# Kernel tuning notes

Measured on AMD Instinct MI355X. Metric: run time of the kernel, lower is better.

## Reference

```python
import math
import jax, jax.numpy as jnp
import numpy as np

D_MODEL = 1024
N_HEADS = 16
D_HEAD = D_MODEL // N_HEADS


def setup_inputs() -> dict:
    key = jax.random.key(0)
    kx, kqkv, ko = jax.random.split(key, 3)
    B, T = 4, 2048
    x = jax.random.normal(kx, (B, T, D_MODEL), dtype=jnp.float32)
    # Linear(d_model, 3*d_model, bias=False): weight stored as [out, in]
    s = 1.0 / math.sqrt(D_MODEL)
    W_qkv = jax.random.uniform(kqkv, (3 * D_MODEL, D_MODEL), dtype=jnp.float32, minval=-s, maxval=s)
    W_o = jax.random.uniform(ko, (D_MODEL, D_MODEL), dtype=jnp.float32, minval=-s, maxval=s)
    return {"x": x, "W_qkv": W_qkv, "W_o": W_o}


def reference(x, W_qkv, W_o):
    B, T, C = x.shape
    H, Dh = N_HEADS, D_HEAD
    qkv = jnp.einsum('btc,oc->bto', x, W_qkv)            # [B,T,3C]
    qkv = qkv.reshape(B, T, 3, H, Dh)
    q = jnp.transpose(qkv[:, :, 0], (0, 2, 1, 3))        # [B,H,T,Dh]
    k = jnp.transpose(qkv[:, :, 1], (0, 2, 1, 3))
    v = jnp.transpose(qkv[:, :, 2], (0, 2, 1, 3))
    scale = 1.0 / math.sqrt(Dh)
    attn = jnp.einsum('bhqd,bhkd->bhqk', q, k) * scale   # [B,H,T,T]
    causal = jnp.tril(jnp.ones((T, T), dtype=bool))
    attn = jnp.where(causal, attn, -jnp.inf)
    attn = jax.nn.softmax(attn, axis=-1)
    out = jnp.einsum('bhqk,bhkd->bhqd', attn, v)         # [B,H,T,Dh]
    out = jnp.transpose(out, (0, 2, 1, 3)).reshape(B, T, C)
    return jnp.einsum('btc,oc->bto', out, W_o)
```

## Files before the change

kernel.cpp:

```cpp
#include <hip/hip_runtime.h>
#include <hip/hip_bf16.h>
#include <cstdint>

#define TT      2048
#define NBATCH  4
#define BTROWS  8192
#define CDIM    1024
#define NQKV    3072
#define QSCALE  0.18033688011112042f

using bf16x8 = __attribute__((ext_vector_type(8))) short;
using f32x4  = __attribute__((ext_vector_type(4))) float;
using f32x16 = __attribute__((ext_vector_type(16))) float;

#define GLOAD_LDS16(g, l)                                                     \
  __builtin_amdgcn_global_load_lds(                                           \
      (const __attribute__((address_space(1))) unsigned int*)(g),             \
      (__attribute__((address_space(3))) unsigned int*)(l), 16, 0, 0)

__device__ inline short f2bf(float f) {
  unsigned u = __builtin_bit_cast(unsigned, f);
  u += 0x7FFF + ((u >> 16) & 1);
  return (short)(u >> 16);
}

__global__ __launch_bounds__(256) void conv_bf16(const float* __restrict__ in,
                                                 short* __restrict__ out, int n) {
  int i = (blockIdx.x * 256 + threadIdx.x) * 4;
  if (i + 3 < n) {
    float4 v = *(const float4*)(in + i);
    short4 o;
    o.x = f2bf(v.x); o.y = f2bf(v.y); o.z = f2bf(v.z); o.w = f2bf(v.w);
    *(short4*)(out + i) = o;
  }
}

__global__ __launch_bounds__(256) void gemm_qkv(const short* __restrict__ A,
                                                const short* __restrict__ Bw,
                                                short* __restrict__ Qb,
                                                short* __restrict__ Kb,
                                                short* __restrict__ Vb) {
  const int K = CDIM;
  __shared__ __attribute__((aligned(16))) short As[128 * 32];
  __shared__ __attribute__((aligned(16))) short Bs[128 * 32];
  int tid = threadIdx.x;
  int bid = blockIdx.x;
  int bm = ((bid & 7) << 3) | (bid >> 3);
  int bn = blockIdx.y;
  int lane = tid & 63, wid = tid >> 6;
  int wr = wid >> 1, wc = wid & 1;
  int la = lane & 15, lg = lane >> 4;

  const short* Ab = A + (size_t)bm * 128 * K;
  const short* Bb = Bw + (size_t)bn * 128 * K;

  f32x4 acc[4][4];
#pragma unroll
  for (int m = 0; m < 4; m++)
#pragma unroll
    for (int n = 0; n < 4; n++) acc[m][n] = (f32x4){0.f, 0.f, 0.f, 0.f};

  int c0 = tid, c1 = tid + 256;
  for (int k0 = 0; k0 < K; k0 += 32) {
    GLOAD_LDS16(Ab + (c0 >> 2) * K + k0 + (c0 & 3) * 8, &As[c0 * 8]);
    GLOAD_LDS16(Ab + (c1 >> 2) * K + k0 + (c1 & 3) * 8, &As[c1 * 8]);
    GLOAD_LDS16(Bb + (c0 >> 2) * K + k0 + (c0 & 3) * 8, &Bs[c0 * 8]);
    GLOAD_LDS16(Bb + (c1 >> 2) * K + k0 + (c1 & 3) * 8, &Bs[c1 * 8]);
    __syncthreads();
    bf16x8 af[4], bfr[4];
#pragma unroll
    for (int m = 0; m < 4; m++)
      af[m] = *(const bf16x8*)&As[(wr * 64 + m * 16 + la) * 32 + lg * 8];
#pragma unroll
    for (int n = 0; n < 4; n++)
      bfr[n] = *(const bf16x8*)&Bs[(wc * 64 + n * 16 + la) * 32 + lg * 8];
#pragma unroll
    for (int m = 0; m < 4; m++)
#pragma unroll
      for (int n = 0; n < 4; n++)
        acc[m][n] = __builtin_amdgcn_mfma_f32_16x16x32_bf16(af[m], bfr[n],
                                                            acc[m][n], 0, 0, 0);
    __syncthreads();
  }

#pragma unroll
  for (int m = 0; m < 4; m++) {
    int rbase = bm * 128 + wr * 64 + m * 16 + lg * 4;
    int b = rbase >> 11;
    int tb = rbase & 2047;
#pragma unroll
    for (int n = 0; n < 4; n++) {
      int col = bn * 128 + wc * 64 + n * 16 + la;
      int which = col >> 10;
      int h = (col >> 6) & 15;
      int d = col & 63;
      if (which == 2) {
        short4 o4;
        o4.x = f2bf(acc[m][n][0]); o4.y = f2bf(acc[m][n][1]);
        o4.z = f2bf(acc[m][n][2]); o4.w = f2bf(acc[m][n][3]);
        *(short4*)&Vb[((size_t)(b * 16 + h) * 64 + d) * TT + tb] = o4;
      } else {
        short* dst = (which == 0) ? Qb : Kb;
        float sc = (which == 0) ? QSCALE : 1.0f;
        size_t base = ((size_t)(b * 16 + h) * TT) * 64 + d;
#pragma unroll
        for (int r = 0; r < 4; r++)
          dst[base + (size_t)(tb + r) * 64] = f2bf(acc[m][n][r] * sc);
      }
    }
  }
}

__global__ __launch_bounds__(256, 3) void attn_fwd2(const short* __restrict__ Qb,
                                                    const short* __restrict__ Kb,
                                                    const short* __restrict__ Vtg,
                                                    short* __restrict__ Ob) {
  __shared__ __attribute__((aligned(16))) short lds[10240];
  short* Ks = lds;
  short* Vs = lds + 4096;

  int tid = threadIdx.x, lane = tid & 63, w = tid >> 6;
  int l31 = lane & 31, hi = lane >> 5, l7 = lane & 7;
  int gid = blockIdx.x;
  int qt = 15 - (gid & 15);
  int bh = gid >> 4;
  int q0 = qt * 128;
  int qw = q0 + w * 32;
  int qg = qw + l31;

  const short* Qh = Qb + (size_t)bh * TT * 64;
  const short* Kh = Kb + (size_t)bh * TT * 64;
  const short* Vh = Vtg + (size_t)bh * 64 * TT;

  bf16x8 q[4];
#pragma unroll
  for (int c = 0; c < 4; c++)
    q[c] = *(const bf16x8*)(Qh + (size_t)qg * 64 + c * 16 + hi * 8);

  f32x16 o0, o1;
#pragma unroll
  for (int r = 0; r < 16; r++) { o0[r] = 0.f; o1[r] = 0.f; }
  float m = -1e30f, lsum = 0.f;

  int nt = 2 * qt + 2;
  int c0 = tid, c1 = tid + 256;
  int r0 = c0 >> 3, cc0 = c0 & 7;
  int r1 = c1 >> 3, cc1 = c1 & 7;

  bf16x8 kr0, kr1, vr0, vr1;
  kr0 = *(const bf16x8*)(Kh + (size_t)r0 * 64 + cc0 * 8);
  kr1 = *(const bf16x8*)(Kh + (size_t)r1 * 64 + cc1 * 8);
  vr0 = *(const bf16x8*)(Vh + (size_t)r0 * TT + cc0 * 8);
  vr1 = *(const bf16x8*)(Vh + (size_t)r1 * TT + cc1 * 8);

  for (int it = 0; it < nt; it++) {
    int kv0 = it * 64;
    __syncthreads();
    *(bf16x8*)&Ks[r0 * 64 + ((cc0 ^ (r0 & 7)) * 8)] = kr0;
    *(bf16x8*)&Ks[r1 * 64 + ((cc1 ^ (r1 & 7)) * 8)] = kr1;
    *(bf16x8*)&Vs[r0 * 64 + ((cc0 ^ (r0 & 7)) * 8)] = vr0;
    *(bf16x8*)&Vs[r1 * 64 + ((cc1 ^ (r1 & 7)) * 8)] = vr1;
    __syncthreads();
    if (it + 1 < nt) {
      int kn = kv0 + 64;
      kr0 = *(const bf16x8*)(Kh + (size_t)(kn + r0) * 64 + cc0 * 8);
      kr1 = *(const bf16x8*)(Kh + (size_t)(kn + r1) * 64 + cc1 * 8);
      vr0 = *(const bf16x8*)(Vh + (size_t)r0 * TT + kn + cc0 * 8);
      vr1 = *(const bf16x8*)(Vh + (size_t)r1 * TT + kn + cc1 * 8);
    }
    if (kv0 <= qw + 31) {
      f32x16 st0, st1;
#pragma unroll
      for (int r = 0; r < 16; r++) { st0[r] = 0.f; st1[r] = 0.f; }
#pragma unroll
      for (int c = 0; c < 4; c++) {
        int cc = c * 2 + hi;
        bf16x8 kf0 = *(const bf16x8*)&Ks[l31 * 64 + ((cc ^ l7) * 8)];
        bf16x8 kf1 = *(const bf16x8*)&Ks[(32 + l31) * 64 + ((cc ^ l7) * 8)];
        st0 = __builtin_amdgcn_mfma_f32_32x32x16_bf16(kf0, q[c], st0, 0, 0, 0);
        st1 = __builtin_amdgcn_mfma_f32_32x32x16_bf16(kf1, q[c], st1, 0, 0, 0);
      }
      if (kv0 + 63 > qw) {
#pragma unroll
        for (int r = 0; r < 16; r++) {
          int kloc = (r & 3) + 8 * (r >> 2) + 4 * hi;
          if (kv0 + kloc > qg)      st0[r] = -1e30f;
          if (kv0 + 32 + kloc > qg) st1[r] = -1e30f;
        }
      }
      float tm[16];
#pragma unroll
      for (int r = 0; r < 16; r++) tm[r] = fmaxf(st0[r], st1[r]);
#pragma unroll
      for (int s = 8; s >= 1; s >>= 1)
#pragma unroll
        for (int r = 0; r < 16; r++)
          if (r < s) tm[r] = fmaxf(tm[r], tm[r + s]);
      float pm = tm[0];
      pm = fmaxf(pm, __shfl_xor(pm, 32));
      if (!__all(pm <= m + 8.f)) {
        float mn = fmaxf(m, pm);
        float fac = exp2f(m - mn);
        lsum *= fac;
#pragma unroll
        for (int r = 0; r < 16; r++) { o0[r] *= fac; o1[r] *= fac; }
        m = mn;
      }
      float ts[16];
#pragma unroll
      for (int r = 0; r < 16; r++) {
        st0[r] = exp2f(st0[r] - m);
        st1[r] = exp2f(st1[r] - m);
        ts[r] = st0[r] + st1[r];
      }
#pragma unroll
      for (int s = 8; s >= 1; s >>= 1)
#pragma unroll
        for (int r = 0; r < 16; r++)
          if (r < s) ts[r] += ts[r + s];
      float rs = ts[0];
      rs += __shfl_xor(rs, 32);
      lsum += rs;
#pragma unroll
      for (int kb = 0; kb < 2; kb++) {
#pragma unroll
        for (int c2 = 0; c2 < 2; c2++) {
          float p0 = kb ? st1[8 * c2 + 0] : st0[8 * c2 + 0];
          float p1 = kb ? st1[8 * c2 + 1] : st0[8 * c2 + 1];
          float p2 = kb ? st1[8 * c2 + 2] : st0[8 * c2 + 2];
          float p3 = kb ? st1[8 * c2 + 3] : st0[8 * c2 + 3];
          float p4 = kb ? st1[8 * c2 + 4] : st0[8 * c2 + 4];
          float p5 = kb ? st1[8 * c2 + 5] : st0[8 * c2 + 5];
          float p6 = kb ? st1[8 * c2 + 6] : st0[8 * c2 + 6];
          float p7 = kb ? st1[8 * c2 + 7] : st0[8 * c2 + 7];
          unsigned u0, u1, u2, u3;
          asm("v_cvt_pk_bf16_f32 %0, %1, %2" : "=v"(u0) : "v"(p0), "v"(p1));
          asm("v_cvt_pk_bf16_f32 %0, %1, %2" : "=v"(u1) : "v"(p2), "v"(p3));
          asm("v_cvt_pk_bf16_f32 %0, %1, %2" : "=v"(u2) : "v"(p4), "v"(p5));
          asm("v_cvt_pk_bf16_f32 %0, %1, %2" : "=v"(u3) : "v"(p6), "v"(p7));
          asm volatile("v_permlane32_swap_b32 %0, %1" : "+v"(u0), "+v"(u2));
          asm volatile("v_permlane32_swap_b32 %0, %1" : "+v"(u1), "+v"(u3));
          union { unsigned u[4]; bf16x8 v; } pa;
          pa.u[0] = u0; pa.u[1] = u1; pa.u[2] = u2; pa.u[3] = u3;
          int ccv = kb * 4 + c2 * 2 + hi;
          bf16x8 vf0 = *(const bf16x8*)&Vs[l31 * 64 + ((ccv ^ l7) * 8)];
          bf16x8 vf1 = *(const bf16x8*)&Vs[(32 + l31) * 64 + ((ccv ^ l7) * 8)];
          o0 = __builtin_amdgcn_mfma_f32_32x32x16_bf16(vf0, pa.v, o0, 0, 0, 0);
          o1 = __builtin_amdgcn_mfma_f32_32x32x16_bf16(vf1, pa.v, o1, 0, 0, 0);
        }
      }
    }
  }

  __syncthreads();
  short* Os = lds + w * (32 * 80);
  float inv = 1.f / lsum;
#pragma unroll
  for (int k = 0; k < 4; k++) {
    float a0 = o0[4 * k + 0] * inv, a1 = o0[4 * k + 1] * inv;
    float a2 = o0[4 * k + 2] * inv, a3 = o0[4 * k + 3] * inv;
    float b0 = o1[4 * k + 0] * inv, b1 = o1[4 * k + 1] * inv;
    float b2 = o1[4 * k + 2] * inv, b3 = o1[4 * k + 3] * inv;
    unsigned w0, w1, w2, w3;
    asm("v_cvt_pk_bf16_f32 %0, %1, %2" : "=v"(w0) : "v"(a0), "v"(a1));
    asm("v_cvt_pk_bf16_f32 %0, %1, %2" : "=v"(w1) : "v"(a2), "v"(a3));
    asm("v_cvt_pk_bf16_f32 %0, %1, %2" : "=v"(w2) : "v"(b0), "v"(b1));
    asm("v_cvt_pk_bf16_f32 %0, %1, %2" : "=v"(w3) : "v"(b2), "v"(b3));
    int d = 8 * k + 4 * hi;
    uint2 pa; pa.x = w0; pa.y = w1;
    uint2 pb; pb.x = w2; pb.y = w3;
    *(uint2*)&Os[l31 * 80 + d] = pa;
    *(uint2*)&Os[l31 * 80 + 32 + d] = pb;
  }
  __syncthreads();
  int b = bh >> 4, h = bh & 15;
#pragma unroll
  for (int pass = 0; pass < 4; pass++) {
    int qr = pass * 8 + (lane >> 3);
    int cc = lane & 7;
    bf16x8 v = *(const bf16x8*)&Os[qr * 80 + cc * 8];
    *(bf16x8*)&Ob[((size_t)(b * TT + q0 + w * 32 + qr)) * CDIM + h * 64 + cc * 8] = v;
  }
}

__global__ __launch_bounds__(256) void gemm_out(const short* __restrict__ A,
                                                const short* __restrict__ Bw,
                                                float* __restrict__ C) {
  const int K = CDIM;
  __shared__ __attribute__((aligned(16))) short As[128 * 32];
  __shared__ __attribute__((aligned(16))) short Bs[128 * 32];
  int tid = threadIdx.x;
  int bid = blockIdx.x;
  int bm = ((bid & 7) << 3) | (bid >> 3);
  int bn = blockIdx.y;
  int lane = tid & 63, wid = tid >> 6;
  int wr = wid >> 1, wc = wid & 1;
  int la = lane & 15, lg = lane >> 4;

  const short* Ab = A + (size_t)bm * 128 * K;
  const short* Bb = Bw + (size_t)bn * 128 * K;

  f32x4 acc[4][4];
#pragma unroll
  for (int m = 0; m < 4; m++)
#pragma unroll
    for (int n = 0; n < 4; n++) acc[m][n] = (f32x4){0.f, 0.f, 0.f, 0.f};

  int c0 = tid, c1 = tid + 256;
  for (int k0 = 0; k0 < K; k0 += 32) {
    GLOAD_LDS16(Ab + (c0 >> 2) * K + k0 + (c0 & 3) * 8, &As[c0 * 8]);
    GLOAD_LDS16(Ab + (c1 >> 2) * K + k0 + (c1 & 3) * 8, &As[c1 * 8]);
    GLOAD_LDS16(Bb + (c0 >> 2) * K + k0 + (c0 & 3) * 8, &Bs[c0 * 8]);
    GLOAD_LDS16(Bb + (c1 >> 2) * K + k0 + (c1 & 3) * 8, &Bs[c1 * 8]);
    __syncthreads();
    bf16x8 af[4], bfr[4];
#pragma unroll
    for (int m = 0; m < 4; m++)
      af[m] = *(const bf16x8*)&As[(wr * 64 + m * 16 + la) * 32 + lg * 8];
#pragma unroll
    for (int n = 0; n < 4; n++)
      bfr[n] = *(const bf16x8*)&Bs[(wc * 64 + n * 16 + la) * 32 + lg * 8];
#pragma unroll
    for (int m = 0; m < 4; m++)
#pragma unroll
      for (int n = 0; n < 4; n++)
        acc[m][n] = __builtin_amdgcn_mfma_f32_16x16x32_bf16(af[m], bfr[n],
                                                            acc[m][n], 0, 0, 0);
    __syncthreads();
  }

#pragma unroll
  for (int m = 0; m < 4; m++) {
    int rbase = bm * 128 + wr * 64 + m * 16 + lg * 4;
#pragma unroll
    for (int n = 0; n < 4; n++) {
      int col = bn * 128 + wc * 64 + n * 16 + la;
#pragma unroll
      for (int r = 0; r < 4; r++)
        C[(size_t)(rbase + r) * CDIM + col] = acc[m][n][r];
    }
  }
}

extern "C" void kernel_launch(void* const* d_in, const int* in_sizes, int n_in,
                              void* d_out, int out_size, void* d_ws, size_t ws_size,
                              hipStream_t stream) {
  const float* x    = (const float*)d_in[0];
  const float* wqkv = (const float*)d_in[1];
  const float* wo   = (const float*)d_in[2];
  float* out = (float*)d_out;

  char* ws = (char*)d_ws;
  short* xb  = (short*)(ws);
  short* wqb = (short*)(ws + (size_t)(16 << 20));
  short* wob = (short*)(ws + (size_t)(22 << 20));
  short* Qb  = (short*)(ws + (size_t)(24 << 20));
  short* Kb  = (short*)(ws + (size_t)(40 << 20));
  short* Vb  = (short*)(ws + (size_t)(56 << 20));
  short* Ob  = (short*)(ws + (size_t)(72 << 20));

  conv_bf16<<<8192, 256, 0, stream>>>(x, xb, BTROWS * CDIM);
  conv_bf16<<<3072, 256, 0, stream>>>(wqkv, wqb, NQKV * CDIM);
  conv_bf16<<<1024, 256, 0, stream>>>(wo, wob, CDIM * CDIM);

  gemm_qkv<<<dim3(BTROWS / 128, NQKV / 128), 256, 0, stream>>>(xb, wqb, Qb, Kb, Vb);
  attn_fwd2<<<NBATCH * 16 * (TT / 128), 256, 0, stream>>>(Qb, Kb, Vb, Ob);
  gemm_out<<<dim3(BTROWS / 128, CDIM / 128), 256, 0, stream>>>(Ob, wob, out);
}
```

Measured before the change: 310.1 us.

## Stage Q/K epilogue through LDS for coalesced stores; raise MFMA wave priority

```diff
diff --git a/kernel.cpp b/kernel.cpp
--- a/kernel.cpp
+++ b/kernel.cpp
@@ -41,8 +41,9 @@
                                                 short* __restrict__ Kb,
                                                 short* __restrict__ Vb) {
   const int K = CDIM;
-  __shared__ __attribute__((aligned(16))) short As[128 * 32];
-  __shared__ __attribute__((aligned(16))) short Bs[128 * 32];
+  __shared__ __attribute__((aligned(16))) short smem[8192];
+  short* As = smem;
+  short* Bs = smem + 4096;
   int tid = threadIdx.x;
   int bid = blockIdx.x;
   int bm = ((bid & 7) << 3) | (bid >> 3);
@@ -83,30 +84,46 @@
     __syncthreads();
   }
 
-#pragma unroll
-  for (int m = 0; m < 4; m++) {
-    int rbase = bm * 128 + wr * 64 + m * 16 + lg * 4;
-    int b = rbase >> 11;
-    int tb = rbase & 2047;
-#pragma unroll
-    for (int n = 0; n < 4; n++) {
-      int col = bn * 128 + wc * 64 + n * 16 + la;
-      int which = col >> 10;
-      int h = (col >> 6) & 15;
-      int d = col & 63;
-      if (which == 2) {
+  int colbase = bn * 128 + wc * 64;
+  int which = colbase >> 10;
+  int b = bm >> 4;
+
+  if (which == 2) {
+#pragma unroll
+    for (int m = 0; m < 4; m++) {
+      int tb = (bm * 128 + wr * 64 + m * 16 + lg * 4) & 2047;
+#pragma unroll
+      for (int n = 0; n < 4; n++) {
+        int col = colbase + n * 16 + la;
+        int h = (col >> 6) & 15;
+        int d = col & 63;
         short4 o4;
         o4.x = f2bf(acc[m][n][0]); o4.y = f2bf(acc[m][n][1]);
         o4.z = f2bf(acc[m][n][2]); o4.w = f2bf(acc[m][n][3]);
         *(short4*)&Vb[((size_t)(b * 16 + h) * 64 + d) * TT + tb] = o4;
-      } else {
-        short* dst = (which == 0) ? Qb : Kb;
-        float sc = (which == 0) ? QSCALE : 1.0f;
-        size_t base = ((size_t)(b * 16 + h) * TT) * 64 + d;
+      }
+    }
+  } else {
+    short* dst = (which == 0) ? Qb : Kb;
+    float sc = (which == 0) ? QSCALE : 1.0f;
+    int h = (colbase >> 6) & 15;
+    size_t hbase = ((size_t)(b * 16 + h) * TT) * 64;
+    short* Ls = smem + wid * (16 * 72);
+    int rrow = lane & 15, chunk = lane >> 4;
+#pragma unroll
+    for (int m = 0; m < 4; m++) {
+#pragma unroll
+      for (int n = 0; n < 4; n++)
 #pragma unroll
         for (int r = 0; r < 4; r++)
-          dst[base + (size_t)(tb + r) * 64] = f2bf(acc[m][n][r] * sc);
-      }
+          Ls[(lg * 4 + r) * 72 + n * 16 + la] = f2bf(acc[m][n][r] * sc);
+      __syncthreads();
+      int t = (bm * 128 + wr * 64 + m * 16 + rrow) & 2047;
+      bf16x8 v0 = *(const bf16x8*)&Ls[rrow * 72 + chunk * 16];
+      bf16x8 v1 = *(const bf16x8*)&Ls[rrow * 72 + chunk * 16 + 8];
+      *(bf16x8*)&dst[hbase + (size_t)t * 64 + chunk * 16] = v0;
+      *(bf16x8*)&dst[hbase + (size_t)t * 64 + chunk * 16 + 8] = v1;
+      __syncthreads();
     }
   }
 }
@@ -172,6 +189,7 @@
       f32x16 st0, st1;
 #pragma unroll
       for (int r = 0; r < 16; r++) { st0[r] = 0.f; st1[r] = 0.f; }
+      __builtin_amdgcn_s_setprio(1);
 #pragma unroll
       for (int c = 0; c < 4; c++) {
         int cc = c * 2 + hi;
@@ -180,6 +198,7 @@
         st0 = __builtin_amdgcn_mfma_f32_32x32x16_bf16(kf0, q[c], st0, 0, 0, 0);
         st1 = __builtin_amdgcn_mfma_f32_32x32x16_bf16(kf1, q[c], st1, 0, 0, 0);
       }
+      __builtin_amdgcn_s_setprio(0);
       if (kv0 + 63 > qw) {
 #pragma unroll
         for (int r = 0; r < 16; r++) {
@@ -221,6 +240,7 @@
       float rs = ts[0];
       rs += __shfl_xor(rs, 32);
       lsum += rs;
+      __builtin_amdgcn_s_setprio(1);
 #pragma unroll
       for (int kb = 0; kb < 2; kb++) {
 #pragma unroll
@@ -249,6 +269,7 @@
           o1 = __builtin_amdgcn_mfma_f32_32x32x16_bf16(vf1, pa.v, o1, 0, 0, 0);
         }
       }
+      __builtin_amdgcn_s_setprio(0);
     }
   }
 
```

Result: no change. 308.2 us (-0.6%).
